# Performance work log

Measured on AMD Instinct MI355X. Metric: run time of the kernel, lower is better.

Reference implementation:

```python
import jax, jax.numpy as jnp
import numpy as np

N, E, IN, TD, H, C0, C1 = 50000, 800000, 128, 64, 4, 64, 16
SLOPE = 0.2


def setup_inputs() -> dict:
    key = jax.random.key(0)
    ks = jax.random.split(key, 20)
    def rn(k, shape, scale=1.0):
        return jax.random.normal(k, shape, dtype=jnp.float32) * scale
    return {
        "x": rn(ks[0], (N, IN)),
        "edge_index": jax.random.randint(ks[1], (2, E), 0, N),
        "timestamps": jax.random.uniform(ks[2], (E,), dtype=jnp.float32),
        # TimeEncoder: linear(1 -> TD) then cos, then abs
        "time_w": rn(ks[3], (TD,)),
        "time_b": rn(ks[4], (TD,)),
        # GATConv layer 0: in=IN, out-per-head=C0, heads=H
        "W0": rn(ks[5], (IN, H * C0), 0.1),
        "att_src0": rn(ks[6], (H, C0), 0.1),
        "att_dst0": rn(ks[7], (H, C0), 0.1),
        "lin_edge0": rn(ks[8], (TD, H * C0), 0.1),
        "att_edge0": rn(ks[9], (H, C0), 0.1),
        "bias0": rn(ks[10], (H * C0,), 0.1),
        # GATConv layer 1: in=H*C0, out-per-head=C1, heads=H
        "W1": rn(ks[11], (H * C0, H * C1), 0.1),
        "att_src1": rn(ks[12], (H, C1), 0.1),
        "att_dst1": rn(ks[13], (H, C1), 0.1),
        "lin_edge1": rn(ks[14], (TD, H * C1), 0.1),
        "att_edge1": rn(ks[15], (H, C1), 0.1),
        "bias1": rn(ks[16], (H * C1,), 0.1),
    }


def gat_layer(h_in, src, dst, edge_attr, W, a_src, a_dst, W_e, a_e, bias):
    """One PyG-style GATConv with edge-attr attention (concat heads, no dropout)."""
    heads = a_src.shape[0]
    HC = W.shape[1]
    C = HC // heads
    n_nodes = h_in.shape[0]
    h = (h_in @ W).reshape(n_nodes, heads, C)                 # [N, H, C]
    e = (edge_attr @ W_e).reshape(-1, heads, C)               # [Et, H, C]
    # attention logits per edge, per head
    alpha = ((h * a_src).sum(-1)[src]
             + (h * a_dst).sum(-1)[dst]
             + (e * a_e).sum(-1))                              # [Et, H]
    alpha = jnp.where(alpha >= 0, alpha, SLOPE * alpha)       # leaky relu
    # segment softmax over destination node
    m = jax.ops.segment_max(alpha, dst, num_segments=n_nodes)  # [N, H]
    ea = jnp.exp(alpha - m[dst])
    s = jax.ops.segment_sum(ea, dst, num_segments=n_nodes)
    a = ea / (s[dst] + 1e-16)                                 # [Et, H]
    # weighted scatter-add aggregation
    out = jax.ops.segment_sum(h[src] * a[..., None], dst, num_segments=n_nodes)
    return out.reshape(n_nodes, HC) + bias


def reference(x, edge_index, timestamps, time_w, time_b,
              W0, att_src0, att_dst0, lin_edge0, att_edge0, bias0,
              W1, att_src1, att_dst1, lin_edge1, att_edge1, bias1):
    # TimeEncoder -> abs, per-edge feature [E, TD]
    ef = jnp.abs(jnp.cos(timestamps[:, None] * time_w + time_b))
    # add self loops with edge_attr fill value 1.0
    loops = jnp.arange(N)
    src = jnp.concatenate([edge_index[0], loops])
    dst = jnp.concatenate([edge_index[1], loops])
    ef = jnp.concatenate([ef, jnp.ones((N, TD), ef.dtype)], axis=0)
    h = gat_layer(x, src, dst, ef, W0, att_src0, att_dst0, lin_edge0, att_edge0, bias0)
    h = gat_layer(h, src, dst, ef, W1, att_src1, att_dst1, lin_edge1, att_edge1, bias1)
    return h  # [N, H*C1] = [50000, 64]
```

## Files before the change

### kernel.cpp

```cpp
#include <hip/hip_runtime.h>
#include <math.h>

#define N_NODES 50000
#define N_EDGES 800000
#define ET (N_EDGES + N_NODES)
#define IN_F 128
#define TDIM 64
#define HEADS 4
#define C0 64
#define C1 16
#define HC0 256
#define HC1 64
#define KF 512
#define SLOPE 0.2f
#define TAB 4096
#define BSHIFT 8
#define NBUCKET 196
#define CHUNK 2048

using short8 = __attribute__((ext_vector_type(8))) short;
using f32x4 = __attribute__((ext_vector_type(4))) float;

__device__ __forceinline__ float bf2f(unsigned u16) { return __uint_as_float(u16 << 16); }
__device__ __forceinline__ unsigned short f2bf(float f) {
    unsigned u = __float_as_uint(f);
    return (unsigned short)((u + 0x7fffu + ((u >> 16) & 1u)) >> 16);
}
__device__ __forceinline__ unsigned pk2(float lo, float hi) {
    return (unsigned)f2bf(lo) | ((unsigned)f2bf(hi) << 16);
}
__device__ __forceinline__ float lrelu(float a) { return a >= 0.f ? a : SLOPE * a; }

__global__ __launch_bounds__(256) void k_param(
    const float* __restrict__ le0, const float* __restrict__ at0, const float* __restrict__ le1,
    const float* __restrict__ at1, const float* __restrict__ W0, const float* __restrict__ asr,
    const float* __restrict__ ads, const float* __restrict__ W1, const float* __restrict__ bias0,
    float* __restrict__ v0, float* __restrict__ v1, float* __restrict__ l0,
    float* __restrict__ l1, float* __restrict__ as0, float* __restrict__ ad0,
    unsigned short* __restrict__ W01t, float* __restrict__ b01) {
    int b = blockIdx.x, tid = threadIdx.x;
    int h = tid >> 6, c = tid & 63;
    if (b < 64) {
        int td = b;
        float p0 = le0[td * HC0 + h * C0 + c] * at0[h * C0 + c];
        for (int m = 1; m < 64; m <<= 1) p0 += __shfl_xor(p0, m);
        if (c == 0) v0[td * 4 + h] = p0;
        float p1 = 0.f;
        if (c < C1) p1 = le1[td * HC1 + h * C1 + c] * at1[h * C1 + c];
        for (int m = 1; m < 16; m <<= 1) p1 += __shfl_xor(p1, m);
        if (c == 0) v1[td * 4 + h] = p1;
    } else if (b == 64) {
        float s0 = 0.f;
        for (int td = 0; td < TDIM; ++td) s0 += le0[td * HC0 + h * C0 + c];
        s0 *= at0[h * C0 + c];
        for (int m = 1; m < 64; m <<= 1) s0 += __shfl_xor(s0, m);
        if (c == 0) l0[h] = s0;
        float s1 = 0.f;
        if (c < C1) {
            for (int td = 0; td < TDIM; ++td) s1 += le1[td * HC1 + h * C1 + c];
            s1 *= at1[h * C1 + c];
        }
        for (int m = 1; m < 16; m <<= 1) s1 += __shfl_xor(s1, m);
        if (c == 0) l1[h] = s1;
    } else if (b < 193) {
        int k = b - 65;
        float wv = W0[k * HC0 + h * C0 + c];
        float ps = wv * asr[h * C0 + c];
        float pd = wv * ads[h * C0 + c];
        for (int m = 1; m < 64; m <<= 1) {
            ps += __shfl_xor(ps, m);
            pd += __shfl_xor(pd, m);
        }
        if (c == 0) {
            as0[h * IN_F + k] = ps;
            ad0[h * IN_F + k] = pd;
        }
    } else if (b < 321) {
        int hk = (b - 193) * 4 + (tid >> 6);
        int c1 = tid & 63;
        int hh = hk >> 7, k = hk & 127;
        float acc = 0.f;
        for (int c0 = 0; c0 < C0; ++c0)
            acc += W0[k * HC0 + hh * C0 + c0] * W1[(size_t)(hh * C0 + c0) * HC1 + c1];
        W01t[(size_t)c1 * KF + hk] = f2bf(acc);
    } else {
        if (tid < 64) {
            float acc = 0.f;
            for (int k = 0; k < HC0; ++k) acc += bias0[k] * W1[(size_t)k * HC1 + tid];
            b01[tid] = acc;
        }
    }
}

__global__ __launch_bounds__(256) void k_aetab(const float* __restrict__ tw,
                                               const float* __restrict__ tb,
                                               const float* __restrict__ v0,
                                               const float* __restrict__ v1,
                                               float* __restrict__ tab0,
                                               float* __restrict__ tab1) {
    __shared__ float sw[TDIM], sb[TDIM], sv0[TDIM * 4], sv1[TDIM * 4];
    int tid = threadIdx.x;
    if (tid < TDIM) {
        sw[tid] = tw[tid];
        sb[tid] = tb[tid];
    }
    sv0[tid] = v0[tid];
    sv1[tid] = v1[tid];
    __syncthreads();
    int i = blockIdx.x * 256 + tid;
    if (i > TAB) return;
    float time = (float)i / (float)TAB;
    float a00 = 0, a01 = 0, a02 = 0, a03 = 0, a10 = 0, a11 = 0, a12 = 0, a13 = 0;
#pragma unroll 8
    for (int d = 0; d < TDIM; ++d) {
        float f = fabsf(__cosf(time * sw[d] + sb[d]));
        a00 += f * sv0[d * 4 + 0];
        a01 += f * sv0[d * 4 + 1];
        a02 += f * sv0[d * 4 + 2];
        a03 += f * sv0[d * 4 + 3];
        a10 += f * sv1[d * 4 + 0];
        a11 += f * sv1[d * 4 + 1];
        a12 += f * sv1[d * 4 + 2];
        a13 += f * sv1[d * 4 + 3];
    }
    ((float4*)tab0)[i] = make_float4(a00, a01, a02, a03);
    ((float4*)tab1)[i] = make_float4(a10, a11, a12, a13);
}

__global__ __launch_bounds__(256) void k_xbs(const float* __restrict__ x,
                                             const float* __restrict__ as0,
                                             const float* __restrict__ ad0,
                                             unsigned short* __restrict__ xb,
                                             float* __restrict__ ssrc, float* __restrict__ sdst) {
    int w = threadIdx.x >> 6, l = threadIdx.x & 63;
    int n = blockIdx.x * 4 + w;
    if (n >= N_NODES) return;
    float2 xv = *(const float2*)(x + (size_t)n * IN_F + l * 2);
    *(unsigned*)(xb + (size_t)n * IN_F + l * 2) = pk2(xv.x, xv.y);
    float ps[4], pd[4];
#pragma unroll
    for (int h = 0; h < 4; ++h) {
        float2 a = *(const float2*)(as0 + h * IN_F + l * 2);
        float2 d = *(const float2*)(ad0 + h * IN_F + l * 2);
        ps[h] = xv.x * a.x + xv.y * a.y;
        pd[h] = xv.x * d.x + xv.y * d.y;
    }
#pragma unroll
    for (int m = 1; m < 64; m <<= 1) {
#pragma unroll
        for (int h = 0; h < 4; ++h) {
            ps[h] += __shfl_xor(ps[h], m);
            pd[h] += __shfl_xor(pd[h], m);
        }
    }
    if (l == 0) {
#pragma unroll
        for (int h = 0; h < 4; ++h) {
            ssrc[n * 4 + h] = ps[h];
            sdst[n * 4 + h] = pd[h];
        }
    }
}

__global__ void k_count(const int* __restrict__ ei, int* __restrict__ deg) {
    int t = blockIdx.x * blockDim.x + threadIdx.x;
    if (t >= N_EDGES) return;
    atomicAdd(&deg[ei[N_EDGES + t]], 1);
}

__global__ void k_scan_block(const int* __restrict__ deg, int* __restrict__ rowptr,
                             int* __restrict__ blocksum, int n) {
    __shared__ int buf[256];
    int tid = threadIdx.x, i = blockIdx.x * 256 + tid;
    int v = (i < n) ? (deg[i] + 1) : 0;
    buf[tid] = v;
    __syncthreads();
    for (int off = 1; off < 256; off <<= 1) {
        int t = (tid >= off) ? buf[tid - off] : 0;
        __syncthreads();
        buf[tid] += t;
        __syncthreads();
    }
    if (i < n) rowptr[i + 1] = buf[tid];
    if (tid == 255) blocksum[blockIdx.x] = buf[255];
}

__global__ void k_scan_top(const int* __restrict__ blocksum, int* __restrict__ blockoff, int nb) {
    __shared__ int buf[256];
    int tid = threadIdx.x;
    int v = (tid < nb) ? blocksum[tid] : 0;
    buf[tid] = v;
    __syncthreads();
    for (int off = 1; off < 256; off <<= 1) {
        int t = (tid >= off) ? buf[tid - off] : 0;
        __syncthreads();
        buf[tid] += t;
        __syncthreads();
    }
    if (tid < nb) blockoff[tid] = buf[tid] - v;
}

__global__ void k_finalize(int* __restrict__ rowptr, const int* __restrict__ blockoff,
                           const int* __restrict__ deg, int* __restrict__ cursor,
                           int* __restrict__ edst, int* __restrict__ esrc,
                           float* __restrict__ tsp, int* __restrict__ bcur) {
    int i = blockIdx.x * 256 + threadIdx.x;
    if (i >= N_NODES) return;
    int v = rowptr[i + 1] + blockoff[blockIdx.x];
    rowptr[i + 1] = v;
    int start = v - deg[i] - 1;
    cursor[i] = start;
    if (i == 0) rowptr[0] = 0;
    if ((i & 255) == 0) bcur[i >> BSHIFT] = start;
    for (int p = start; p < v; ++p) edst[p] = i;
    esrc[v - 1] = i;
    tsp[v - 1] = -1.f;
}

__global__ __launch_bounds__(256) void k_bucketA(const int* __restrict__ ei,
                                                 const float* __restrict__ ts,
                                                 int* __restrict__ bcur,
                                                 int4* __restrict__ staging) {
    __shared__ int cnt[NBUCKET], base[NBUCKET];
    int tid = threadIdx.x;
    int e0 = blockIdx.x * CHUNK;
    for (int i = tid; i < NBUCKET; i += 256) cnt[i] = 0;
    __syncthreads();
    int s[8], d[8], tv[8];
#pragma unroll
    for (int i = 0; i < 8; ++i) {
        int tt = e0 + i * 256 + tid;
        if (tt < N_EDGES) {
            s[i] = ei[tt];
            d[i] = ei[N_EDGES + tt];
            tv[i] = __float_as_int(ts[tt]);
            atomicAdd(&cnt[d[i] >> BSHIFT], 1);
        } else {
            d[i] = -1;
        }
    }
    __syncthreads();
    for (int i = tid; i < NBUCKET; i += 256) {
        int c = cnt[i];
        base[i] = c ? atomicAdd(&bcur[i], c) : 0;
        cnt[i] = 0;
    }
    __syncthreads();
#pragma unroll
    for (int i = 0; i < 8; ++i) {
        if (d[i] >= 0) {
            int b = d[i] >> BSHIFT;
            int off = atomicAdd(&cnt[b], 1);
            staging[base[b] + off] = make_int4(s[i], d[i], tv[i], 0);
        }
    }
}

__global__ __launch_bounds__(256) void k_bucketB(const int* __restrict__ rowptr,
                                                 const int* __restrict__ bcur,
                                                 const int4* __restrict__ staging,
                                                 int* __restrict__ cursor,
                                                 int* __restrict__ esrc,
                                                 float* __restrict__ tsp) {
    int b = blockIdx.x;
    int lo = rowptr[b << BSHIFT];
    int hi = bcur[b];
    for (int p = lo + threadIdx.x; p < hi; p += 256) {
        int4 sdt = staging[p];
        int q = atomicAdd(&cursor[sdt.y], 1);
        esrc[q] = sdt.x;
        tsp[q] = __int_as_float(sdt.z);
    }
}

__global__ void k_expand(const int* __restrict__ esrc, const int* __restrict__ edst,
                         const float* __restrict__ tsp, const float* __restrict__ tab0,
                         const float* __restrict__ l0, const float* __restrict__ ssrc0,
                         const float* __restrict__ sdst0, float* __restrict__ ew0p) {
    int p = blockIdx.x * blockDim.x + threadIdx.x;
    if (p >= ET) return;
    float tv = tsp[p];
    float4 a0;
    if (tv < 0.f) {
        a0 = ((const float4*)l0)[0];
    } else {
        float f = tv * (float)TAB;
        int i = (int)f;
        i = i > TAB - 1 ? TAB - 1 : i;
        float fr = f - (float)i;
        float4 t0 = ((const float4*)tab0)[i];
        float4 t1 = ((const float4*)tab0)[i + 1];
        a0.x = t0.x + fr * (t1.x - t0.x);
        a0.y = t0.y + fr * (t1.y - t0.y);
        a0.z = t0.z + fr * (t1.z - t0.z);
        a0.w = t0.w + fr * (t1.w - t0.w);
    }
    int s = esrc[p], d = edst[p];
    float4 sv = ((const float4*)ssrc0)[s];
    float4 dv = ((const float4*)sdst0)[d];
    float4 w;
    w.x = __expf(lrelu(sv.x + dv.x + a0.x));
    w.y = __expf(lrelu(sv.y + dv.y + a0.y));
    w.z = __expf(lrelu(sv.z + dv.z + a0.z));
    w.w = __expf(lrelu(sv.w + dv.w + a0.w));
    ((float4*)ew0p)[p] = w;
}

__global__ void k_ew1(const int* __restrict__ esrc, const int* __restrict__ edst,
                      const float* __restrict__ tsp, const float* __restrict__ tab1,
                      const float* __restrict__ l1, const float* __restrict__ ssrc,
                      const float* __restrict__ sdst, float* __restrict__ ew1p) {
    int p = blockIdx.x * blockDim.x + threadIdx.x;
    if (p >= ET) return;
    float tv = tsp[p];
    float4 av;
    if (tv < 0.f) {
        av = ((const float4*)l1)[0];
    } else {
        float f = tv * (float)TAB;
        int i = (int)f;
        i = i > TAB - 1 ? TAB - 1 : i;
        float fr = f - (float)i;
        float4 t0 = ((const float4*)tab1)[i];
        float4 t1 = ((const float4*)tab1)[i + 1];
        av.x = t0.x + fr * (t1.x - t0.x);
        av.y = t0.y + fr * (t1.y - t0.y);
        av.z = t0.z + fr * (t1.z - t0.z);
        av.w = t0.w + fr * (t1.w - t0.w);
    }
    int s = esrc[p], d = edst[p];
    float4 sv = ((const float4*)ssrc)[s];
    float4 dv = ((const float4*)sdst)[d];
    float4 w;
    w.x = __expf(lrelu(sv.x + dv.x + av.x));
    w.y = __expf(lrelu(sv.y + dv.y + av.y));
    w.z = __expf(lrelu(sv.z + dv.z + av.z));
    w.w = __expf(lrelu(sv.w + dv.w + av.w));
    ((float4*)ew1p)[p] = w;
}

__global__ __launch_bounds__(256) void k_aggx(const unsigned short* __restrict__ xb,
                                              const int* __restrict__ esrc,
                                              const float* __restrict__ ew0p,
                                              const int* __restrict__ rowptr,
                                              unsigned short* __restrict__ aggx) {
    int grp = threadIdx.x >> 4, lo = threadIdx.x & 15;
    int n = blockIdx.x * 16 + grp;
    if (n >= N_NODES) return;
    int p0 = rowptr[n], p1 = rowptr[n + 1];
    float acc[4][8];
#pragma unroll
    for (int h = 0; h < 4; ++h)
#pragma unroll
        for (int j = 0; j < 8; ++j) acc[h][j] = 0.f;
    float ss0 = 0, ss1 = 0, ss2 = 0, ss3 = 0;
    float4 e_cur = ((const float4*)ew0p)[p0];
    uint4 x_cur = *(const uint4*)(xb + (size_t)esrc[p0] * IN_F + lo * 8);
    int s_nxt = (p0 + 1 < p1) ? esrc[p0 + 1] : 0;
    for (int p = p0; p < p1; ++p) {
        float4 e = e_cur;
        uint4 xv = x_cur;
        if (p + 1 < p1) {
            e_cur = ((const float4*)ew0p)[p + 1];
            x_cur = *(const uint4*)(xb + (size_t)s_nxt * IN_F + lo * 8);
            if (p + 2 < p1) s_nxt = esrc[p + 2];
        }
        float f[8];
        f[0] = bf2f(xv.x & 0xffff);
        f[1] = bf2f(xv.x >> 16);
        f[2] = bf2f(xv.y & 0xffff);
        f[3] = bf2f(xv.y >> 16);
        f[4] = bf2f(xv.z & 0xffff);
        f[5] = bf2f(xv.z >> 16);
        f[6] = bf2f(xv.w & 0xffff);
        f[7] = bf2f(xv.w >> 16);
#pragma unroll
        for (int j = 0; j < 8; ++j) {
            acc[0][j] += e.x * f[j];
            acc[1][j] += e.y * f[j];
            acc[2][j] += e.z * f[j];
            acc[3][j] += e.w * f[j];
        }
        ss0 += e.x;
        ss1 += e.y;
        ss2 += e.z;
        ss3 += e.w;
    }
    float inv[4] = {1.f / (ss0 + 1e-16f), 1.f / (ss1 + 1e-16f), 1.f / (ss2 + 1e-16f),
                    1.f / (ss3 + 1e-16f)};
    size_t base = (size_t)n * KF + lo * 8;
#pragma unroll
    for (int h = 0; h < 4; ++h) {
        uint4 r;
        r.x = pk2(acc[h][0] * inv[h], acc[h][1] * inv[h]);
        r.y = pk2(acc[h][2] * inv[h], acc[h][3] * inv[h]);
        r.z = pk2(acc[h][4] * inv[h], acc[h][5] * inv[h]);
        r.w = pk2(acc[h][6] * inv[h], acc[h][7] * inv[h]);
        *(uint4*)(aggx + base + h * IN_F) = r;
    }
}

__global__ __launch_bounds__(256) void k_gemm1s(
    const unsigned short* __restrict__ A, const unsigned short* __restrict__ Bt,
    const float* __restrict__ b01, const float* __restrict__ a_src,
    const float* __restrict__ a_dst, unsigned short* __restrict__ h1b, float* __restrict__ ssrc,
    float* __restrict__ sdst) {
    __shared__ unsigned short As[128 * 40];
    __shared__ unsigned short Bs[64 * 40];
    int tid = threadIdx.x, w = tid >> 6, l = tid & 63, lo = l & 15, hi = l >> 4;
    int m0 = blockIdx.x * 128;
    f32x4 acc[2][4];
#pragma unroll
    for (int i = 0; i < 2; ++i)
#pragma unroll
        for (int j = 0; j < 4; ++j) acc[i][j] = (f32x4){0.f, 0.f, 0.f, 0.f};
    int arow4 = tid >> 2, aseg = tid & 3;
    for (int k0 = 0; k0 < KF; k0 += 32) {
#pragma unroll
        for (int hf = 0; hf < 2; ++hf) {
            int arow = hf * 64 + arow4;
            uint4 va = {0, 0, 0, 0};
            if (m0 + arow < N_NODES)
                va = *(const uint4*)(A + (size_t)(m0 + arow) * KF + k0 + aseg * 8);
            *(uint4*)&As[arow * 40 + aseg * 8] = va;
        }
        uint4 vb = *(const uint4*)(Bt + (size_t)arow4 * KF + k0 + aseg * 8);
        *(uint4*)&Bs[arow4 * 40 + aseg * 8] = vb;
        __syncthreads();
        short8 af[2], bf[4];
#pragma unroll
        for (int fa = 0; fa < 2; ++fa)
            af[fa] = *(const short8*)&As[(w * 32 + fa * 16 + lo) * 40 + hi * 8];
#pragma unroll
        for (int nf = 0; nf < 4; ++nf) bf[nf] = *(const short8*)&Bs[(nf * 16 + lo) * 40 + hi * 8];
#pragma unroll
        for (int fa = 0; fa < 2; ++fa)
#pragma unroll
            for (int nf = 0; nf < 4; ++nf)
                acc[fa][nf] =
                    __builtin_amdgcn_mfma_f32_16x16x32_bf16(af[fa], bf[nf], acc[fa][nf], 0, 0, 0);
        __syncthreads();
    }
    float asv[4], adv[4], bv[4];
#pragma unroll
    for (int nf = 0; nf < 4; ++nf) {
        asv[nf] = a_src[nf * 16 + lo];
        adv[nf] = a_dst[nf * 16 + lo];
        bv[nf] = b01[nf * 16 + lo];
    }
#pragma unroll
    for (int fa = 0; fa < 2; ++fa)
#pragma unroll
        for (int r = 0; r < 4; ++r) {
            int row = m0 + w * 32 + fa * 16 + hi * 4 + r;
#pragma unroll
            for (int nf = 0; nf < 4; ++nf) {
                float v = acc[fa][nf][r] + bv[nf];
                if (row < N_NODES) h1b[(size_t)row * HC1 + nf * 16 + lo] = f2bf(v);
                float ps = v * asv[nf], pd = v * adv[nf];
                for (int m = 1; m < 16; m <<= 1) {
                    ps += __shfl_xor(ps, m);
                    pd += __shfl_xor(pd, m);
                }
                if (lo == 0 && row < N_NODES) {
                    ssrc[row * 4 + nf] = ps;
                    sdst[row * 4 + nf] = pd;
                }
            }
        }
}

__global__ __launch_bounds__(256) void k_agg1(
    const unsigned short* __restrict__ h1b, const int* __restrict__ esrc,
    const float* __restrict__ ew1p, const int* __restrict__ rowptr,
    const float* __restrict__ bias, float* __restrict__ out) {
    int grp = threadIdx.x >> 4, lo = threadIdx.x & 15;
    int n = blockIdx.x * 16 + grp;
    if (n >= N_NODES) return;
    int head = lo >> 2;
    int p0 = rowptr[n], p1 = rowptr[n + 1];
    float a0 = 0, a1 = 0, a2 = 0, a3 = 0, ss = 0;
    float e_cur = ew1p[p0 * 4 + head];
    uint2 h_cur = *(const uint2*)(h1b + (size_t)esrc[p0] * HC1 + lo * 4);
    for (int p = p0; p < p1; ++p) {
        float e = e_cur;
        uint2 hv = h_cur;
        if (p + 1 < p1) {
            e_cur = ew1p[(p + 1) * 4 + head];
            h_cur = *(const uint2*)(h1b + (size_t)esrc[p + 1] * HC1 + lo * 4);
        }
        a0 += e * bf2f(hv.x & 0xffff);
        a1 += e * bf2f(hv.x >> 16);
        a2 += e * bf2f(hv.y & 0xffff);
        a3 += e * bf2f(hv.y >> 16);
        ss += e;
    }
    float inv = 1.f / (ss + 1e-16f);
    float4 b4 = *(const float4*)(bias + lo * 4);
    float4 r = make_float4(a0 * inv + b4.x, a1 * inv + b4.y, a2 * inv + b4.z, a3 * inv + b4.w);
    *(float4*)(out + (size_t)n * HC1 + lo * 4) = r;
}

extern "C" void kernel_launch(void* const* d_in, const int* in_sizes, int n_in, void* d_out,
                              int out_size, void* d_ws, size_t ws_size, hipStream_t stream) {
    const float* x = (const float*)d_in[0];
    const int* ei = (const int*)d_in[1];
    const float* ts = (const float*)d_in[2];
    const float* time_w = (const float*)d_in[3];
    const float* time_b = (const float*)d_in[4];
    const float* W0 = (const float*)d_in[5];
    const float* att_src0 = (const float*)d_in[6];
    const float* att_dst0 = (const float*)d_in[7];
    const float* lin_edge0 = (const float*)d_in[8];
    const float* att_edge0 = (const float*)d_in[9];
    const float* bias0 = (const float*)d_in[10];
    const float* W1 = (const float*)d_in[11];
    const float* att_src1 = (const float*)d_in[12];
    const float* att_dst1 = (const float*)d_in[13];
    const float* lin_edge1 = (const float*)d_in[14];
    const float* att_edge1 = (const float*)d_in[15];
    const float* bias1 = (const float*)d_in[16];
    float* out = (float*)d_out;

    char* ws = (char*)d_ws;
    size_t off = 0;
    auto alloc = [&](size_t bytes) -> void* {
        void* p = ws + off;
        off = (off + bytes + 255) & ~(size_t)255;
        return p;
    };
    unsigned short* xb = (unsigned short*)alloc((size_t)N_NODES * IN_F * 2);
    unsigned short* aggx = (unsigned short*)alloc((size_t)N_NODES * KF * 2);
    unsigned short* h1b = (unsigned short*)alloc((size_t)N_NODES * HC1 * 2);
    unsigned short* W01t = (unsigned short*)alloc((size_t)HC1 * KF * 2);
    float* b01 = (float*)alloc(HC1 * 4);
    float* as0 = (float*)alloc(4 * IN_F * 4);
    float* ad0 = (float*)alloc(4 * IN_F * 4);
    float* tab0 = (float*)alloc((size_t)(TAB + 1) * 4 * 4);
    float* tab1 = (float*)alloc((size_t)(TAB + 1) * 4 * 4);
    float* ew0p = (float*)alloc((size_t)ET * 4 * 4);
    float* ew1p = (float*)alloc((size_t)ET * 4 * 4);
    float* ssrc0 = (float*)alloc((size_t)N_NODES * 4 * 4);
    float* sdst0 = (float*)alloc((size_t)N_NODES * 4 * 4);
    float* ssrc1 = (float*)alloc((size_t)N_NODES * 4 * 4);
    float* sdst1 = (float*)alloc((size_t)N_NODES * 4 * 4);
    float* v0 = (float*)alloc(TDIM * 4 * 4);
    float* v1 = (float*)alloc(TDIM * 4 * 4);
    float* l0 = (float*)alloc(16);
    float* l1 = (float*)alloc(16);
    float* tsp = (float*)alloc((size_t)ET * 4);
    int* deg = (int*)alloc((size_t)N_NODES * 4);
    int* rowptr = (int*)alloc((size_t)(N_NODES + 1) * 4);
    int* cursor = (int*)alloc((size_t)(N_NODES + 1) * 4);
    int* blocksum = (int*)alloc(256 * 4);
    int* blockoff = (int*)alloc(256 * 4);
    int* bcur = (int*)alloc(NBUCKET * 4);
    int4* staging = (int4*)alloc((size_t)ET * 16);
    int* esrc = (int*)alloc((size_t)ET * 4);
    int* edst = (int*)alloc((size_t)ET * 4);
    (void)ws_size;
    (void)in_sizes;
    (void)n_in;
    (void)out_size;

    int nb = (N_NODES + 255) / 256;
    int ebks = (ET + 255) / 256;
    int rbks = (N_EDGES + 255) / 256;
    int cbks = (N_EDGES + CHUNK - 1) / CHUNK;
    int gx = (N_NODES + 127) / 128;
    int nblk16 = (N_NODES + 15) / 16;
    int nblk4 = (N_NODES + 3) / 4;

    k_param<<<322, 256, 0, stream>>>(lin_edge0, att_edge0, lin_edge1, att_edge1, W0, att_src0,
                                     att_dst0, W1, bias0, v0, v1, l0, l1, as0, ad0, W01t, b01);
    k_aetab<<<(TAB + 256) / 256, 256, 0, stream>>>(time_w, time_b, v0, v1, tab0, tab1);

    k_xbs<<<nblk4, 256, 0, stream>>>(x, as0, ad0, xb, ssrc0, sdst0);

    hipMemsetAsync(deg, 0, (size_t)N_NODES * 4, stream);
    k_count<<<rbks, 256, 0, stream>>>(ei, deg);
    k_scan_block<<<nb, 256, 0, stream>>>(deg, rowptr, blocksum, N_NODES);
    k_scan_top<<<1, 256, 0, stream>>>(blocksum, blockoff, nb);
    k_finalize<<<nb, 256, 0, stream>>>(rowptr, blockoff, deg, cursor, edst, esrc, tsp, bcur);
    k_bucketA<<<cbks, 256, 0, stream>>>(ei, ts, bcur, staging);
    k_bucketB<<<NBUCKET, 256, 0, stream>>>(rowptr, bcur, staging, cursor, esrc, tsp);

    k_expand<<<ebks, 256, 0, stream>>>(esrc, edst, tsp, tab0, l0, ssrc0, sdst0, ew0p);

    k_aggx<<<nblk16, 256, 0, stream>>>(xb, esrc, ew0p, rowptr, aggx);

    k_gemm1s<<<gx, 256, 0, stream>>>(aggx, W01t, b01, att_src1, att_dst1, h1b, ssrc1, sdst1);
    k_ew1<<<ebks, 256, 0, stream>>>(esrc, edst, tsp, tab1, l1, ssrc1, sdst1, ew1p);
    k_agg1<<<nblk16, 256, 0, stream>>>(h1b, esrc, ew1p, rowptr, bias1, out);
}
```

Measured before the change: 247.7 us.

## Fuse edge-weight, table and degree-reset work into existing kernels; precompute layer-1 scores algebraically

Merges the time-encoding table build into the parameter kernel and folds the degree reset into the x-conversion kernel. The layer-0 edge-weight expansion now happens in the bucket scatter and finalize kernels, so a separate pass over all edges is removed. Layer-1 source and destination attention scores are computed in the aggregation kernel from precomputed projected vectors, which strips the shuffle-reduction epilogue from the GEMM. Bucket size is halved to give the scatter kernel more blocks. The cost is more divergent, heavier work inside the scatter and aggregation kernels.

After: 262.7 us. 6.1% more time.

```diff
diff --git a/kernel.cpp b/kernel.cpp
--- a/kernel.cpp
+++ b/kernel.cpp
@@ -14,8 +14,8 @@
 #define KF 512
 #define SLOPE 0.2f
 #define TAB 4096
-#define BSHIFT 8
-#define NBUCKET 196
+#define BSHIFT 7
+#define NBUCKET 391
 #define CHUNK 2048
 
 using short8 = __attribute__((ext_vector_type(8))) short;
@@ -35,21 +35,15 @@
     const float* __restrict__ le0, const float* __restrict__ at0, const float* __restrict__ le1,
     const float* __restrict__ at1, const float* __restrict__ W0, const float* __restrict__ asr,
     const float* __restrict__ ads, const float* __restrict__ W1, const float* __restrict__ bias0,
-    float* __restrict__ v0, float* __restrict__ v1, float* __restrict__ l0,
+    const float* __restrict__ asr1, const float* __restrict__ ads1,
+    const float* __restrict__ tw, const float* __restrict__ tb, float* __restrict__ l0,
     float* __restrict__ l1, float* __restrict__ as0, float* __restrict__ ad0,
-    unsigned short* __restrict__ W01t, float* __restrict__ b01) {
+    unsigned short* __restrict__ W01t, float* __restrict__ b01, float* __restrict__ as1,
+    float* __restrict__ ad1, float* __restrict__ bs1, float* __restrict__ bd1,
+    float* __restrict__ tab0, float* __restrict__ tab1) {
     int b = blockIdx.x, tid = threadIdx.x;
     int h = tid >> 6, c = tid & 63;
-    if (b < 64) {
-        int td = b;
-        float p0 = le0[td * HC0 + h * C0 + c] * at0[h * C0 + c];
-        for (int m = 1; m < 64; m <<= 1) p0 += __shfl_xor(p0, m);
-        if (c == 0) v0[td * 4 + h] = p0;
-        float p1 = 0.f;
-        if (c < C1) p1 = le1[td * HC1 + h * C1 + c] * at1[h * C1 + c];
-        for (int m = 1; m < 16; m <<= 1) p1 += __shfl_xor(p1, m);
-        if (c == 0) v1[td * 4 + h] = p1;
-    } else if (b == 64) {
+    if (b == 0) {
         float s0 = 0.f;
         for (int td = 0; td < TDIM; ++td) s0 += le0[td * HC0 + h * C0 + c];
         s0 *= at0[h * C0 + c];
@@ -62,8 +56,8 @@
         }
         for (int m = 1; m < 16; m <<= 1) s1 += __shfl_xor(s1, m);
         if (c == 0) l1[h] = s1;
-    } else if (b < 193) {
-        int k = b - 65;
+    } else if (b < 129) {
+        int k = b - 1;
         float wv = W0[k * HC0 + h * C0 + c];
         float ps = wv * asr[h * C0 + c];
         float pd = wv * ads[h * C0 + c];
@@ -75,63 +69,85 @@
             as0[h * IN_F + k] = ps;
             ad0[h * IN_F + k] = pd;
         }
-    } else if (b < 321) {
-        int hk = (b - 193) * 4 + (tid >> 6);
+    } else if (b < 257) {
+        int hk = (b - 129) * 4 + (tid >> 6);
         int c1 = tid & 63;
         int hh = hk >> 7, k = hk & 127;
         float acc = 0.f;
         for (int c0 = 0; c0 < C0; ++c0)
             acc += W0[k * HC0 + hh * C0 + c0] * W1[(size_t)(hh * C0 + c0) * HC1 + c1];
         W01t[(size_t)c1 * KF + hk] = f2bf(acc);
-    } else {
+        float ps = acc * asr1[c1];
+        float pd = acc * ads1[c1];
+        for (int m = 1; m < 16; m <<= 1) {
+            ps += __shfl_xor(ps, m);
+            pd += __shfl_xor(pd, m);
+        }
+        if ((c1 & 15) == 0) {
+            as1[(c1 >> 4) * KF + hk] = ps;
+            ad1[(c1 >> 4) * KF + hk] = pd;
+        }
+    } else if (b == 257) {
         if (tid < 64) {
             float acc = 0.f;
             for (int k = 0; k < HC0; ++k) acc += bias0[k] * W1[(size_t)k * HC1 + tid];
             b01[tid] = acc;
-        }
-    }
-}
-
-__global__ __launch_bounds__(256) void k_aetab(const float* __restrict__ tw,
-                                               const float* __restrict__ tb,
-                                               const float* __restrict__ v0,
-                                               const float* __restrict__ v1,
-                                               float* __restrict__ tab0,
-                                               float* __restrict__ tab1) {
-    __shared__ float sw[TDIM], sb[TDIM], sv0[TDIM * 4], sv1[TDIM * 4];
-    int tid = threadIdx.x;
-    if (tid < TDIM) {
-        sw[tid] = tw[tid];
-        sb[tid] = tb[tid];
-    }
-    sv0[tid] = v0[tid];
-    sv1[tid] = v1[tid];
-    __syncthreads();
-    int i = blockIdx.x * 256 + tid;
-    if (i > TAB) return;
-    float time = (float)i / (float)TAB;
-    float a00 = 0, a01 = 0, a02 = 0, a03 = 0, a10 = 0, a11 = 0, a12 = 0, a13 = 0;
+            float ps = acc * asr1[tid];
+            float pd = acc * ads1[tid];
+            for (int m = 1; m < 16; m <<= 1) {
+                ps += __shfl_xor(ps, m);
+                pd += __shfl_xor(pd, m);
+            }
+            if ((tid & 15) == 0) {
+                bs1[tid >> 4] = ps;
+                bd1[tid >> 4] = pd;
+            }
+        }
+    } else {
+        __shared__ float sv0[TDIM * 4], sv1[TDIM * 4], sw[TDIM], sb[TDIM];
+        int td = tid >> 2, hh = tid & 3;
+        float v0l = 0.f;
+        for (int c0 = 0; c0 < C0; ++c0) v0l += le0[td * HC0 + hh * C0 + c0] * at0[hh * C0 + c0];
+        sv0[td * 4 + hh] = v0l;
+        float v1l = 0.f;
+        for (int c0 = 0; c0 < C1; ++c0) v1l += le1[td * HC1 + hh * C1 + c0] * at1[hh * C1 + c0];
+        sv1[td * 4 + hh] = v1l;
+        if (tid < TDIM) {
+            sw[tid] = tw[tid];
+            sb[tid] = tb[tid];
+        }
+        __syncthreads();
+        int i = (b - 258) * 256 + tid;
+        if (i > TAB) return;
+        float time = (float)i / (float)TAB;
+        float a00 = 0, a01 = 0, a02 = 0, a03 = 0, a10 = 0, a11 = 0, a12 = 0, a13 = 0;
 #pragma unroll 8
-    for (int d = 0; d < TDIM; ++d) {
-        float f = fabsf(__cosf(time * sw[d] + sb[d]));
-        a00 += f * sv0[d * 4 + 0];
-        a01 += f * sv0[d * 4 + 1];
-        a02 += f * sv0[d * 4 + 2];
-        a03 += f * sv0[d * 4 + 3];
-        a10 += f * sv1[d * 4 + 0];
-        a11 += f * sv1[d * 4 + 1];
-        a12 += f * sv1[d * 4 + 2];
-        a13 += f * sv1[d * 4 + 3];
-    }
-    ((float4*)tab0)[i] = make_float4(a00, a01, a02, a03);
-    ((float4*)tab1)[i] = make_float4(a10, a11, a12, a13);
+        for (int d = 0; d < TDIM; ++d) {
+            float f = fabsf(__cosf(time * sw[d] + sb[d]));
+            a00 += f * sv0[d * 4 + 0];
+            a01 += f * sv0[d * 4 + 1];
+            a02 += f * sv0[d * 4 + 2];
+            a03 += f * sv0[d * 4 + 3];
+            a10 += f * sv1[d * 4 + 0];
+            a11 += f * sv1[d * 4 + 1];
+            a12 += f * sv1[d * 4 + 2];
+            a13 += f * sv1[d * 4 + 3];
+        }
+        ((float4*)tab0)[i] = make_float4(a00, a01, a02, a03);
+        ((float4*)tab1)[i] = make_float4(a10, a11, a12, a13);
+    }
 }
 
 __global__ __launch_bounds__(256) void k_xbs(const float* __restrict__ x,
                                              const float* __restrict__ as0,
                                              const float* __restrict__ ad0,
                                              unsigned short* __restrict__ xb,
-                                             float* __restrict__ ssrc, float* __restrict__ sdst) {
+                                             float* __restrict__ ssrc, float* __restrict__ sdst,
+                                             int* __restrict__ deg) {
+    if (blockIdx.x < 196) {
+        int i = blockIdx.x * 256 + threadIdx.x;
+        if (i < N_NODES) deg[i] = 0;
+    }
     int w = threadIdx.x >> 6, l = threadIdx.x & 63;
     int n = blockIdx.x * 4 + w;
     if (n >= N_NODES) return;
@@ -203,7 +219,9 @@
 __global__ void k_finalize(int* __restrict__ rowptr, const int* __restrict__ blockoff,
                            const int* __restrict__ deg, int* __restrict__ cursor,
                            int* __restrict__ edst, int* __restrict__ esrc,
-                           float* __restrict__ tsp, int* __restrict__ bcur) {
+                           float* __restrict__ tsp, int* __restrict__ bcur,
+                           const float* __restrict__ ssrc0, const float* __restrict__ sdst0,
+                           const float* __restrict__ l0, float* __restrict__ ew0p) {
     int i = blockIdx.x * 256 + threadIdx.x;
     if (i >= N_NODES) return;
     int v = rowptr[i + 1] + blockoff[blockIdx.x];
@@ -211,10 +229,19 @@
     int start = v - deg[i] - 1;
     cursor[i] = start;
     if (i == 0) rowptr[0] = 0;
-    if ((i & 255) == 0) bcur[i >> BSHIFT] = start;
+    if ((i & ((1 << BSHIFT) - 1)) == 0) bcur[i >> BSHIFT] = start;
     for (int p = start; p < v; ++p) edst[p] = i;
     esrc[v - 1] = i;
     tsp[v - 1] = -1.f;
+    float4 lv = ((const float4*)l0)[0];
+    float4 sv = ((const float4*)ssrc0)[i];
+    float4 dv = ((const float4*)sdst0)[i];
+    float4 w;
+    w.x = __expf(lrelu(sv.x + dv.x + lv.x));
+    w.y = __expf(lrelu(sv.y + dv.y + lv.y));
+    w.z = __expf(lrelu(sv.z + dv.z + lv.z));
+    w.w = __expf(lrelu(sv.w + dv.w + lv.w));
+    ((float4*)ew0p)[v - 1] = w;
 }
 
 __global__ __launch_bounds__(256) void k_bucketA(const int* __restrict__ ei,
@@ -256,12 +283,11 @@
     }
 }
 
-__global__ __launch_bounds__(256) void k_bucketB(const int* __restrict__ rowptr,
-                                                 const int* __restrict__ bcur,
-                                                 const int4* __restrict__ staging,
-                                                 int* __restrict__ cursor,
-                                                 int* __restrict__ esrc,
-                                                 float* __restrict__ tsp) {
+__global__ __launch_bounds__(256) void k_bucketB(
+    const int* __restrict__ rowptr, const int* __restrict__ bcur,
+    const int4* __restrict__ staging, int* __restrict__ cursor, int* __restrict__ esrc,
+    float* __restrict__ tsp, const float* __restrict__ ssrc0, const float* __restrict__ sdst0,
+    const float* __restrict__ tab0, float* __restrict__ ew0p) {
     int b = blockIdx.x;
     int lo = rowptr[b << BSHIFT];
     int hi = bcur[b];
@@ -269,41 +295,23 @@
         int4 sdt = staging[p];
         int q = atomicAdd(&cursor[sdt.y], 1);
         esrc[q] = sdt.x;
-        tsp[q] = __int_as_float(sdt.z);
-    }
-}
-
-__global__ void k_expand(const int* __restrict__ esrc, const int* __restrict__ edst,
-                         const float* __restrict__ tsp, const float* __restrict__ tab0,
-                         const float* __restrict__ l0, const float* __restrict__ ssrc0,
-                         const float* __restrict__ sdst0, float* __restrict__ ew0p) {
-    int p = blockIdx.x * blockDim.x + threadIdx.x;
-    if (p >= ET) return;
-    float tv = tsp[p];
-    float4 a0;
-    if (tv < 0.f) {
-        a0 = ((const float4*)l0)[0];
-    } else {
+        float tv = __int_as_float(sdt.z);
+        tsp[q] = tv;
         float f = tv * (float)TAB;
         int i = (int)f;
         i = i > TAB - 1 ? TAB - 1 : i;
         float fr = f - (float)i;
         float4 t0 = ((const float4*)tab0)[i];
         float4 t1 = ((const float4*)tab0)[i + 1];
-        a0.x = t0.x + fr * (t1.x - t0.x);
-        a0.y = t0.y + fr * (t1.y - t0.y);
-        a0.z = t0.z + fr * (t1.z - t0.z);
-        a0.w = t0.w + fr * (t1.w - t0.w);
-    }
-    int s = esrc[p], d = edst[p];
-    float4 sv = ((const float4*)ssrc0)[s];
-    float4 dv = ((const float4*)sdst0)[d];
-    float4 w;
-    w.x = __expf(lrelu(sv.x + dv.x + a0.x));
-    w.y = __expf(lrelu(sv.y + dv.y + a0.y));
-    w.z = __expf(lrelu(sv.z + dv.z + a0.z));
-    w.w = __expf(lrelu(sv.w + dv.w + a0.w));
-    ((float4*)ew0p)[p] = w;
+        float4 sv = ((const float4*)ssrc0)[sdt.x];
+        float4 dv = ((const float4*)sdst0)[sdt.y];
+        float4 w;
+        w.x = __expf(lrelu(sv.x + dv.x + t0.x + fr * (t1.x - t0.x)));
+        w.y = __expf(lrelu(sv.y + dv.y + t0.y + fr * (t1.y - t0.y)));
+        w.z = __expf(lrelu(sv.z + dv.z + t0.z + fr * (t1.z - t0.z)));
+        w.w = __expf(lrelu(sv.w + dv.w + t0.w + fr * (t1.w - t0.w)));
+        ((float4*)ew0p)[q] = w;
+    }
 }
 
 __global__ void k_ew1(const int* __restrict__ esrc, const int* __restrict__ edst,
@@ -339,11 +347,12 @@
     ((float4*)ew1p)[p] = w;
 }
 
-__global__ __launch_bounds__(256) void k_aggx(const unsigned short* __restrict__ xb,
-                                              const int* __restrict__ esrc,
-                                              const float* __restrict__ ew0p,
-                                              const int* __restrict__ rowptr,
-                                              unsigned short* __restrict__ aggx) {
+__global__ __launch_bounds__(256) void k_aggx(
+    const unsigned short* __restrict__ xb, const int* __restrict__ esrc,
+    const float* __restrict__ ew0p, const int* __restrict__ rowptr,
+    const float* __restrict__ as1, const float* __restrict__ ad1,
+    const float* __restrict__ bs1, const float* __restrict__ bd1,
+    unsigned short* __restrict__ aggx, float* __restrict__ ssrc1, float* __restrict__ sdst1) {
     int grp = threadIdx.x >> 4, lo = threadIdx.x & 15;
     int n = blockIdx.x * 16 + grp;
     if (n >= N_NODES) return;
@@ -389,22 +398,52 @@
     float inv[4] = {1.f / (ss0 + 1e-16f), 1.f / (ss1 + 1e-16f), 1.f / (ss2 + 1e-16f),
                     1.f / (ss3 + 1e-16f)};
     size_t base = (size_t)n * KF + lo * 8;
+    float ps[4] = {0, 0, 0, 0}, pd[4] = {0, 0, 0, 0};
 #pragma unroll
     for (int h = 0; h < 4; ++h) {
+        float av[8];
+#pragma unroll
+        for (int j = 0; j < 8; ++j) av[j] = acc[h][j] * inv[h];
         uint4 r;
-        r.x = pk2(acc[h][0] * inv[h], acc[h][1] * inv[h]);
-        r.y = pk2(acc[h][2] * inv[h], acc[h][3] * inv[h]);
-        r.z = pk2(acc[h][4] * inv[h], acc[h][5] * inv[h]);
-        r.w = pk2(acc[h][6] * inv[h], acc[h][7] * inv[h]);
+        r.x = pk2(av[0], av[1]);
+        r.y = pk2(av[2], av[3]);
+        r.z = pk2(av[4], av[5]);
+        r.w = pk2(av[6], av[7]);
         *(uint4*)(aggx + base + h * IN_F) = r;
-    }
-}
-
-__global__ __launch_bounds__(256) void k_gemm1s(
-    const unsigned short* __restrict__ A, const unsigned short* __restrict__ Bt,
-    const float* __restrict__ b01, const float* __restrict__ a_src,
-    const float* __restrict__ a_dst, unsigned short* __restrict__ h1b, float* __restrict__ ssrc,
-    float* __restrict__ sdst) {
+        int hkb = h * IN_F + lo * 8;
+#pragma unroll
+        for (int hs = 0; hs < 4; ++hs) {
+            float4 a0 = *(const float4*)(as1 + hs * KF + hkb);
+            float4 a1 = *(const float4*)(as1 + hs * KF + hkb + 4);
+            float4 d0 = *(const float4*)(ad1 + hs * KF + hkb);
+            float4 d1 = *(const float4*)(ad1 + hs * KF + hkb + 4);
+            ps[hs] += av[0] * a0.x + av[1] * a0.y + av[2] * a0.z + av[3] * a0.w + av[4] * a1.x +
+                      av[5] * a1.y + av[6] * a1.z + av[7] * a1.w;
+            pd[hs] += av[0] * d0.x + av[1] * d0.y + av[2] * d0.z + av[3] * d0.w + av[4] * d1.x +
+                      av[5] * d1.y + av[6] * d1.z + av[7] * d1.w;
+        }
+    }
+#pragma unroll
+    for (int m = 1; m < 16; m <<= 1) {
+#pragma unroll
+        for (int hs = 0; hs < 4; ++hs) {
+            ps[hs] += __shfl_xor(ps[hs], m);
+            pd[hs] += __shfl_xor(pd[hs], m);
+        }
+    }
+    if (lo == 0) {
+#pragma unroll
+        for (int hs = 0; hs < 4; ++hs) {
+            ssrc1[n * 4 + hs] = ps[hs] + bs1[hs];
+            sdst1[n * 4 + hs] = pd[hs] + bd1[hs];
+        }
+    }
+}
+
+__global__ __launch_bounds__(256) void k_gemm1(const unsigned short* __restrict__ A,
+                                               const unsigned short* __restrict__ Bt,
+                                               const float* __restrict__ b01,
+                                               unsigned short* __restrict__ h1b) {
     __shared__ unsigned short As[128 * 40];
     __shared__ unsigned short Bs[64 * 40];
     int tid = threadIdx.x, w = tid >> 6, l = tid & 63, lo = l & 15, hi = l >> 4;
@@ -441,31 +480,16 @@
                     __builtin_amdgcn_mfma_f32_16x16x32_bf16(af[fa], bf[nf], acc[fa][nf], 0, 0, 0);
         __syncthreads();
     }
-    float asv[4], adv[4], bv[4];
-#pragma unroll
-    for (int nf = 0; nf < 4; ++nf) {
-        asv[nf] = a_src[nf * 16 + lo];
-        adv[nf] = a_dst[nf * 16 + lo];
-        bv[nf] = b01[nf * 16 + lo];
-    }
 #pragma unroll
     for (int fa = 0; fa < 2; ++fa)
 #pragma unroll
-        for (int r = 0; r < 4; ++r) {
-            int row = m0 + w * 32 + fa * 16 + hi * 4 + r;
-#pragma unroll
-            for (int nf = 0; nf < 4; ++nf) {
-                float v = acc[fa][nf][r] + bv[nf];
-                if (row < N_NODES) h1b[(size_t)row * HC1 + nf * 16 + lo] = f2bf(v);
-                float ps = v * asv[nf], pd = v * adv[nf];
-                for (int m = 1; m < 16; m <<= 1) {
-                    ps += __shfl_xor(ps, m);
-                    pd += __shfl_xor(pd, m);
-                }
-                if (lo == 0 && row < N_NODES) {
-                    ssrc[row * 4 + nf] = ps;
-                    sdst[row * 4 + nf] = pd;
-                }
+        for (int nf = 0; nf < 4; ++nf) {
+            int col = nf * 16 + lo;
+            float bv = b01[col];
+#pragma unroll
+            for (int r = 0; r < 4; ++r) {
+                int row = m0 + w * 32 + fa * 16 + hi * 4 + r;
+                if (row < N_NODES) h1b[(size_t)row * HC1 + col] = f2bf(acc[fa][nf][r] + bv);
             }
         }
 }
@@ -536,6 +560,10 @@
     float* b01 = (float*)alloc(HC1 * 4);
     float* as0 = (float*)alloc(4 * IN_F * 4);
     float* ad0 = (float*)alloc(4 * IN_F * 4);
+    float* as1 = (float*)alloc(4 * KF * 4);
+    float* ad1 = (float*)alloc(4 * KF * 4);
+    float* bs1 = (float*)alloc(16);
+    float* bd1 = (float*)alloc(16);
     float* tab0 = (float*)alloc((size_t)(TAB + 1) * 4 * 4);
     float* tab1 = (float*)alloc((size_t)(TAB + 1) * 4 * 4);
     float* ew0p = (float*)alloc((size_t)ET * 4 * 4);
@@ -544,8 +572,6 @@
     float* sdst0 = (float*)alloc((size_t)N_NODES * 4 * 4);
     float* ssrc1 = (float*)alloc((size_t)N_NODES * 4 * 4);
     float* sdst1 = (float*)alloc((size_t)N_NODES * 4 * 4);
-    float* v0 = (float*)alloc(TDIM * 4 * 4);
-    float* v1 = (float*)alloc(TDIM * 4 * 4);
     float* l0 = (float*)alloc(16);
     float* l1 = (float*)alloc(16);
     float* tsp = (float*)alloc((size_t)ET * 4);
@@ -571,25 +597,25 @@
     int nblk16 = (N_NODES + 15) / 16;
     int nblk4 = (N_NODES + 3) / 4;
 
-    k_param<<<322, 256, 0, stream>>>(lin_edge0, att_edge0, lin_edge1, att_edge1, W0, att_src0,
-                                     att_dst0, W1, bias0, v0, v1, l0, l1, as0, ad0, W01t, b01);
-    k_aetab<<<(TAB + 256) / 256, 256, 0, stream>>>(time_w, time_b, v0, v1, tab0, tab1);
-
-    k_xbs<<<nblk4, 256, 0, stream>>>(x, as0, ad0, xb, ssrc0, sdst0);
-
-    hipMemsetAsync(deg, 0, (size_t)N_NODES * 4, stream);
+    k_param<<<275, 256, 0, stream>>>(lin_edge0, att_edge0, lin_edge1, att_edge1, W0, att_src0,
+                                     att_dst0, W1, bias0, att_src1, att_dst1, time_w, time_b, l0,
+                                     l1, as0, ad0, W01t, b01, as1, ad1, bs1, bd1, tab0, tab1);
+
+    k_xbs<<<nblk4, 256, 0, stream>>>(x, as0, ad0, xb, ssrc0, sdst0, deg);
+
     k_count<<<rbks, 256, 0, stream>>>(ei, deg);
     k_scan_block<<<nb, 256, 0, stream>>>(deg, rowptr, blocksum, N_NODES);
     k_scan_top<<<1, 256, 0, stream>>>(blocksum, blockoff, nb);
-    k_finalize<<<nb, 256, 0, stream>>>(rowptr, blockoff, deg, cursor, edst, esrc, tsp, bcur);
+    k_finalize<<<nb, 256, 0, stream>>>(rowptr, blockoff, deg, cursor, edst, esrc, tsp, bcur,
+                                       ssrc0, sdst0, l0, ew0p);
     k_bucketA<<<cbks, 256, 0, stream>>>(ei, ts, bcur, staging);
-    k_bucketB<<<NBUCKET, 256, 0, stream>>>(rowptr, bcur, staging, cursor, esrc, tsp);
-
-    k_expand<<<ebks, 256, 0, stream>>>(esrc, edst, tsp, tab0, l0, ssrc0, sdst0, ew0p);
-
-    k_aggx<<<nblk16, 256, 0, stream>>>(xb, esrc, ew0p, rowptr, aggx);
-
-    k_gemm1s<<<gx, 256, 0, stream>>>(aggx, W01t, b01, att_src1, att_dst1, h1b, ssrc1, sdst1);
+    k_bucketB<<<NBUCKET, 256, 0, stream>>>(rowptr, bcur, staging, cursor, esrc, tsp, ssrc0, sdst0,
+                                           tab0, ew0p);
+
+    k_aggx<<<nblk16, 256, 0, stream>>>(xb, esrc, ew0p, rowptr, as1, ad1, bs1, bd1, aggx, ssrc1,
+                                       sdst1);
+
     k_ew1<<<ebks, 256, 0, stream>>>(esrc, edst, tsp, tab1, l1, ssrc1, sdst1, ew1p);
+    k_gemm1<<<gx, 256, 0, stream>>>(aggx, W01t, b01, h1b);
     k_agg1<<<nblk16, 256, 0, stream>>>(h1b, esrc, ew1p, rowptr, bias1, out);
 }
```
